# Optimization experiments

Hardware: AMD Instinct MI355X
Metric: run time of the kernel (lower is better)

The kernel has to match this reference:

```python
import jax, jax.numpy as jnp
import numpy as np

N = 33554432  # 2**25 activations, 128 MB fp32
K = 1024      # winners kept


def setup_inputs() -> dict:
    key = jax.random.key(0)
    inputs = jax.random.normal(key, (N,), dtype=jnp.float32)
    return {"inputs": inputs, "k": K}


def reference(inputs, k):
    # k-th largest value = threshold (original: tf.sort desc, take element k-1)
    topk_vals, _ = jax.lax.top_k(inputs, k)
    threshold = topk_vals[k - 1]
    # zero out everything strictly below the threshold
    return jnp.where(inputs < threshold, jnp.zeros_like(inputs), inputs)
```

## Files before the change

### kernel.cpp

```cpp
#include <hip/hip_runtime.h>
#include <stdint.h>


#define FILTER_KEY 0xC0600000u


typedef float f32x4 __attribute__((ext_vector_type(4)));

__device__ __forceinline__ uint32_t f2key(float x) {
  uint32_t u = __float_as_uint(x);
  return (u & 0x80000000u) ? ~u : (u | 0x80000000u);
}
__device__ __forceinline__ float key2f(uint32_t k) {
  uint32_t u = (k & 0x80000000u) ? (k & 0x7fffffffu) : ~k;
  return __uint_as_float(u);
}

__device__ __forceinline__ void push_cand(uint32_t kk, uint32_t idx,
                                          uint32_t* ctrl, uint32_t* keysA,
                                          uint32_t* idxsA, uint32_t capA) {
  uint32_t p = atomicAdd(&ctrl[0], 1u);
  if (p < capA) { keysA[p] = kk; idxsA[p] = idx; }
}

__global__ void __launch_bounds__(256) k_filter(
    const f32x4* __restrict__ in, int n4, int ntail,
    const float* __restrict__ in_s, uint32_t* __restrict__ ctrl,
    uint32_t* __restrict__ keysA, uint32_t* __restrict__ idxsA,
    uint32_t capA) {
  int gsz = gridDim.x * blockDim.x;
  int i = blockIdx.x * blockDim.x + threadIdx.x;
  for (; i + 7 * gsz < n4; i += 8 * gsz) {
    f32x4 v0 = in[i];
    f32x4 v1 = in[i + gsz];
    f32x4 v2 = in[i + 2 * gsz];
    f32x4 v3 = in[i + 3 * gsz];
    f32x4 v4 = in[i + 4 * gsz];
    f32x4 v5 = in[i + 5 * gsz];
    f32x4 v6 = in[i + 6 * gsz];
    f32x4 v7 = in[i + 7 * gsz];
#define CHECK4(vv, base)                                                       \
    {                                                                          \
      uint32_t k0 = f2key((vv).x), k1 = f2key((vv).y), k2 = f2key((vv).z),     \
               k3 = f2key((vv).w);                                             \
      if (k0 >= FILTER_KEY) push_cand(k0, (base) + 0u, ctrl, keysA, idxsA, capA); \
      if (k1 >= FILTER_KEY) push_cand(k1, (base) + 1u, ctrl, keysA, idxsA, capA); \
      if (k2 >= FILTER_KEY) push_cand(k2, (base) + 2u, ctrl, keysA, idxsA, capA); \
      if (k3 >= FILTER_KEY) push_cand(k3, (base) + 3u, ctrl, keysA, idxsA, capA); \
    }
    CHECK4(v0, 4u * (uint32_t)(i))
    CHECK4(v1, 4u * (uint32_t)(i + gsz))
    CHECK4(v2, 4u * (uint32_t)(i + 2 * gsz))
    CHECK4(v3, 4u * (uint32_t)(i + 3 * gsz))
    CHECK4(v4, 4u * (uint32_t)(i + 4 * gsz))
    CHECK4(v5, 4u * (uint32_t)(i + 5 * gsz))
    CHECK4(v6, 4u * (uint32_t)(i + 6 * gsz))
    CHECK4(v7, 4u * (uint32_t)(i + 7 * gsz))
  }
  for (; i < n4; i += gsz) {
    f32x4 v = in[i];
    CHECK4(v, 4u * (uint32_t)i)
  }
#undef CHECK4
  if (blockIdx.x == 0 && (int)threadIdx.x < ntail) {
    int j = n4 * 4 + threadIdx.x;
    uint32_t kk = f2key(in_s[j]);
    if (kk >= FILTER_KEY) push_cand(kk, (uint32_t)j, ctrl, keysA, idxsA, capA);
  }
}

__global__ void __launch_bounds__(256) k_gather_all(
    const float4* __restrict__ in, int n4, int ntail,
    const float* __restrict__ in_s, const int* __restrict__ kptr,
    uint32_t* __restrict__ ctrl, uint32_t* __restrict__ keysB,
    uint32_t* __restrict__ idxsB, uint32_t capA, uint32_t capB) {
  uint32_t K = (uint32_t)kptr[0];
  uint32_t nA = ctrl[0];
  if (nA >= K && nA <= capA) return;
  int stride = gridDim.x * blockDim.x;
  for (int i = blockIdx.x * blockDim.x + threadIdx.x; i < n4; i += stride) {
    float4 v = in[i];
    uint32_t kk[4] = {f2key(v.x), f2key(v.y), f2key(v.z), f2key(v.w)};
    uint32_t p = atomicAdd(&ctrl[7], 4u);
    for (int c = 0; c < 4; c++)
      if (p + c < capB) { keysB[p + c] = kk[c]; idxsB[p + c] = 4u * (uint32_t)i + c; }
  }
  if (blockIdx.x == 0 && (int)threadIdx.x < ntail) {
    int j = n4 * 4 + threadIdx.x;
    uint32_t p = atomicAdd(&ctrl[7], 1u);
    if (p < capB) { keysB[p] = f2key(in_s[j]); idxsB[p] = (uint32_t)j; }
  }
}

__global__ void __launch_bounds__(1024) k_final(
    const int* __restrict__ kptr, uint32_t* __restrict__ ctrl,
    const uint32_t* __restrict__ keysA, const uint32_t* __restrict__ idxsA,
    uint32_t capA, const uint32_t* __restrict__ keysB,
    const uint32_t* __restrict__ idxsB, uint32_t capB,
    float* __restrict__ out_s) {
  __shared__ uint32_t sh[16384];
  __shared__ uint32_t cnt[16];
  __shared__ uint32_t s_p, s_want;
  int t = threadIdx.x;
  uint32_t K = (uint32_t)kptr[0];
  uint32_t nA = ctrl[0];
  bool useA = (nA >= K && nA <= capA);
  const uint32_t* keys = useA ? keysA : keysB;
  const uint32_t* idxs = useA ? idxsA : idxsB;
  uint32_t n = useA ? nA : ctrl[7];
  if (!useA && n > capB) n = capB;
  bool useLds = (n <= 16384);
  if (useLds) for (uint32_t i = t; i < n; i += blockDim.x) sh[i] = keys[i];
  if (t == 0) { s_p = 0u; s_want = K; }
  __syncthreads();
  uint32_t p = s_p;
  for (int d = 7; d >= 0; d--) {
    if (t < 16) cnt[t] = 0;
    __syncthreads();
    int sh_hi = 4 * d + 4;
    uint32_t pref = (sh_hi < 32) ? (p >> sh_hi) : 0u;
    for (uint32_t i = t; i < n; i += blockDim.x) {
      uint32_t kk = useLds ? sh[i] : keys[i];
      uint32_t hi = (sh_hi < 32) ? (kk >> sh_hi) : 0u;
      if (hi == pref) atomicAdd(&cnt[(kk >> (4 * d)) & 15u], 1u);
    }
    __syncthreads();
    if (t == 0) {
      uint32_t want = s_want, acc = 0, v = 0;
      for (int x = 15; x >= 0; x--) {
        if (acc + cnt[x] >= want) { v = (uint32_t)x; break; }
        acc += cnt[x];
      }
      s_p = p | (v << (4 * d));
      s_want = want - acc;
    }
    __syncthreads();
    p = s_p;
  }
  if (t == 0) ctrl[3] = __float_as_uint(key2f(p));
  for (uint32_t i = t; i < n; i += blockDim.x) {
    uint32_t kk = useLds ? sh[i] : keys[i];
    if (kk >= p) out_s[idxs[i]] = key2f(kk);
  }
}

extern "C" void kernel_launch(void* const* d_in, const int* in_sizes, int n_in,
                              void* d_out, int out_size, void* d_ws, size_t ws_size,
                              hipStream_t stream) {
  const float* in = (const float*)d_in[0];
  const int* kptr = (const int*)d_in[1];
  float* out = (float*)d_out;
  int n = in_sizes[0];
  int n4 = n >> 2;
  int ntail = n & 3;

  uint32_t* ws = (uint32_t*)d_ws;
  uint32_t* ctrl = ws;
  size_t ws_words = ws_size / 4;
  size_t avail = (ws_words > 16) ? (ws_words - 16) : 0;
  uint32_t capA = (uint32_t)((avail / 4 < (1u << 20)) ? avail / 4 : (1u << 20));
  uint32_t* keysA = ws + 16;
  uint32_t* idxsA = keysA + capA;
  size_t availB = avail - 2 * (size_t)capA;
  uint32_t capB = (uint32_t)(availB / 2);
  uint32_t* keysB = idxsA + capA;
  uint32_t* idxsB = keysB + capB;

  hipMemsetAsync(d_ws, 0, 16 * sizeof(uint32_t), stream);
  hipMemsetAsync(d_out, 0, (size_t)out_size, stream);

  k_filter<<<4096, 256, 0, stream>>>((const f32x4*)in, n4, ntail, in,
                                     ctrl, keysA, idxsA, capA);
  k_gather_all<<<2048, 256, 0, stream>>>((const float4*)in, n4, ntail, in,
                                         kptr, ctrl, keysB, idxsB, capA, capB);
  k_final<<<1, 1024, 0, stream>>>(kptr, ctrl, keysA, idxsA, capA,
                                  keysB, idxsB, capB, out);
}
```

Before: 301.8 us.

## Stash filter candidates in registers and flush once per thread with tiled loads

The filter kernel stops issuing one global atomic per candidate. Each thread now keeps up to four candidates in registers and reserves their output slots with a single batched atomicAdd at the end. The input is walked in contiguous 8192-vector tiles per block, and the grid shrinks to 1024 blocks. If any thread sees more than four candidates it raises an overflow flag in ctrl[8], which makes the later kernels fall back to the full gather path. That fallback is a correctness safety net but is very costly if it ever triggers.

```diff
diff --git a/kernel.cpp b/kernel.cpp
--- a/kernel.cpp
+++ b/kernel.cpp
@@ -3,6 +3,7 @@
 
 
 #define FILTER_KEY 0xC0600000u
+#define TILE 8192
 
 
 typedef float f32x4 __attribute__((ext_vector_type(4)));
@@ -14,13 +15,6 @@
 __device__ __forceinline__ float key2f(uint32_t k) {
   uint32_t u = (k & 0x80000000u) ? (k & 0x7fffffffu) : ~k;
   return __uint_as_float(u);
-}
-
-__device__ __forceinline__ void push_cand(uint32_t kk, uint32_t idx,
-                                          uint32_t* ctrl, uint32_t* keysA,
-                                          uint32_t* idxsA, uint32_t capA) {
-  uint32_t p = atomicAdd(&ctrl[0], 1u);
-  if (p < capA) { keysA[p] = kk; idxsA[p] = idx; }
 }
 
 __global__ void __launch_bounds__(256) k_filter(
@@ -28,44 +22,78 @@
     const float* __restrict__ in_s, uint32_t* __restrict__ ctrl,
     uint32_t* __restrict__ keysA, uint32_t* __restrict__ idxsA,
     uint32_t capA) {
-  int gsz = gridDim.x * blockDim.x;
-  int i = blockIdx.x * blockDim.x + threadIdx.x;
-  for (; i + 7 * gsz < n4; i += 8 * gsz) {
-    f32x4 v0 = in[i];
-    f32x4 v1 = in[i + gsz];
-    f32x4 v2 = in[i + 2 * gsz];
-    f32x4 v3 = in[i + 3 * gsz];
-    f32x4 v4 = in[i + 4 * gsz];
-    f32x4 v5 = in[i + 5 * gsz];
-    f32x4 v6 = in[i + 6 * gsz];
-    f32x4 v7 = in[i + 7 * gsz];
-#define CHECK4(vv, base)                                                       \
-    {                                                                          \
-      uint32_t k0 = f2key((vv).x), k1 = f2key((vv).y), k2 = f2key((vv).z),     \
-               k3 = f2key((vv).w);                                             \
-      if (k0 >= FILTER_KEY) push_cand(k0, (base) + 0u, ctrl, keysA, idxsA, capA); \
-      if (k1 >= FILTER_KEY) push_cand(k1, (base) + 1u, ctrl, keysA, idxsA, capA); \
-      if (k2 >= FILTER_KEY) push_cand(k2, (base) + 2u, ctrl, keysA, idxsA, capA); \
-      if (k3 >= FILTER_KEY) push_cand(k3, (base) + 3u, ctrl, keysA, idxsA, capA); \
-    }
-    CHECK4(v0, 4u * (uint32_t)(i))
-    CHECK4(v1, 4u * (uint32_t)(i + gsz))
-    CHECK4(v2, 4u * (uint32_t)(i + 2 * gsz))
-    CHECK4(v3, 4u * (uint32_t)(i + 3 * gsz))
-    CHECK4(v4, 4u * (uint32_t)(i + 4 * gsz))
-    CHECK4(v5, 4u * (uint32_t)(i + 5 * gsz))
-    CHECK4(v6, 4u * (uint32_t)(i + 6 * gsz))
-    CHECK4(v7, 4u * (uint32_t)(i + 7 * gsz))
-  }
-  for (; i < n4; i += gsz) {
-    f32x4 v = in[i];
-    CHECK4(v, 4u * (uint32_t)i)
+  int t = threadIdx.x;
+  uint32_t cnt = 0;
+  uint32_t rk0 = 0, rk1 = 0, rk2 = 0, rk3 = 0;
+  uint32_t ri0 = 0, ri1 = 0, ri2 = 0, ri3 = 0;
+
+#define STASH(kk, idx)                                                      \
+  {                                                                         \
+    if ((kk) >= FILTER_KEY) {                                               \
+      if (cnt == 0)      { rk0 = (kk); ri0 = (idx); }                       \
+      else if (cnt == 1) { rk1 = (kk); ri1 = (idx); }                       \
+      else if (cnt == 2) { rk2 = (kk); ri2 = (idx); }                       \
+      else if (cnt == 3) { rk3 = (kk); ri3 = (idx); }                       \
+      cnt++;                                                                \
+    }                                                                       \
+  }
+#define CHECK4(vv, base)                                                    \
+  {                                                                         \
+    uint32_t c0 = f2key((vv).x), c1 = f2key((vv).y), c2 = f2key((vv).z),    \
+             c3 = f2key((vv).w);                                            \
+    STASH(c0, (base) + 0u)                                                  \
+    STASH(c1, (base) + 1u)                                                  \
+    STASH(c2, (base) + 2u)                                                  \
+    STASH(c3, (base) + 3u)                                                  \
+  }
+
+  int nfull = n4 / TILE;
+  for (int tb = blockIdx.x; tb < nfull; tb += gridDim.x) {
+    const f32x4* p = in + (size_t)tb * TILE;
+    uint32_t tbase = (uint32_t)tb * (TILE * 4u);
+#pragma unroll
+    for (int j = 0; j < TILE / (256 * 8); ++j) {
+      int o = j * 2048 + t;
+      f32x4 v0 = p[o];
+      f32x4 v1 = p[o + 256];
+      f32x4 v2 = p[o + 512];
+      f32x4 v3 = p[o + 768];
+      f32x4 v4 = p[o + 1024];
+      f32x4 v5 = p[o + 1280];
+      f32x4 v6 = p[o + 1536];
+      f32x4 v7 = p[o + 1792];
+      CHECK4(v0, tbase + 4u * (uint32_t)(o))
+      CHECK4(v1, tbase + 4u * (uint32_t)(o + 256))
+      CHECK4(v2, tbase + 4u * (uint32_t)(o + 512))
+      CHECK4(v3, tbase + 4u * (uint32_t)(o + 768))
+      CHECK4(v4, tbase + 4u * (uint32_t)(o + 1024))
+      CHECK4(v5, tbase + 4u * (uint32_t)(o + 1280))
+      CHECK4(v6, tbase + 4u * (uint32_t)(o + 1536))
+      CHECK4(v7, tbase + 4u * (uint32_t)(o + 1792))
+    }
+  }
+  if (blockIdx.x == 0) {
+    for (int i = nfull * TILE + t; i < n4; i += 256) {
+      f32x4 v = in[i];
+      CHECK4(v, 4u * (uint32_t)i)
+    }
+    if ((int)threadIdx.x < ntail) {
+      int j = n4 * 4 + threadIdx.x;
+      uint32_t kk = f2key(in_s[j]);
+      STASH(kk, (uint32_t)j)
+    }
   }
 #undef CHECK4
-  if (blockIdx.x == 0 && (int)threadIdx.x < ntail) {
-    int j = n4 * 4 + threadIdx.x;
-    uint32_t kk = f2key(in_s[j]);
-    if (kk >= FILTER_KEY) push_cand(kk, (uint32_t)j, ctrl, keysA, idxsA, capA);
+#undef STASH
+
+  if (cnt > 4u) ctrl[8] = 1u;
+  uint32_t c = cnt > 4u ? 4u : cnt;
+  if (c) {
+    uint32_t p = atomicAdd(&ctrl[0], c);
+    if (p < capA)     { keysA[p] = rk0;     idxsA[p] = ri0; }
+    if (c > 1 && p + 1 < capA) { keysA[p + 1] = rk1; idxsA[p + 1] = ri1; }
+    if (c > 2 && p + 2 < capA) { keysA[p + 2] = rk2; idxsA[p + 2] = ri2; }
+    if (c > 3 && p + 3 < capA) { keysA[p + 3] = rk3; idxsA[p + 3] = ri3; }
   }
 }
 
@@ -76,7 +104,8 @@
     uint32_t* __restrict__ idxsB, uint32_t capA, uint32_t capB) {
   uint32_t K = (uint32_t)kptr[0];
   uint32_t nA = ctrl[0];
-  if (nA >= K && nA <= capA) return;
+  bool ok = (nA >= K) && (nA <= capA) && (ctrl[8] == 0u);
+  if (ok) return;
   int stride = gridDim.x * blockDim.x;
   for (int i = blockIdx.x * blockDim.x + threadIdx.x; i < n4; i += stride) {
     float4 v = in[i];
@@ -104,7 +133,7 @@
   int t = threadIdx.x;
   uint32_t K = (uint32_t)kptr[0];
   uint32_t nA = ctrl[0];
-  bool useA = (nA >= K && nA <= capA);
+  bool useA = (nA >= K) && (nA <= capA) && (ctrl[8] == 0u);
   const uint32_t* keys = useA ? keysA : keysB;
   const uint32_t* idxs = useA ? idxsA : idxsB;
   uint32_t n = useA ? nA : ctrl[7];
@@ -169,7 +198,7 @@
   hipMemsetAsync(d_ws, 0, 16 * sizeof(uint32_t), stream);
   hipMemsetAsync(d_out, 0, (size_t)out_size, stream);
 
-  k_filter<<<4096, 256, 0, stream>>>((const f32x4*)in, n4, ntail, in,
+  k_filter<<<1024, 256, 0, stream>>>((const f32x4*)in, n4, ntail, in,
                                      ctrl, keysA, idxsA, capA);
   k_gather_all<<<2048, 256, 0, stream>>>((const float4*)in, n4, ntail, in,
                                          kptr, ctrl, keysB, idxsB, capA, capB);
```

Measured after the change: 279.7 us. 1.08x faster.
